# Performance work log

Hardware: AMD Instinct MI355X
Metric: run time of the kernel (lower is better)

The kernel has to match this reference:

```python
import jax, jax.numpy as jnp
import numpy as np

B, S, E, H = 2, 2048, 1024, 16
D = E // H  # head_dim = 64


def setup_inputs() -> dict:
    key = jax.random.key(0)
    k1, k2, k3 = jax.random.split(key, 3)
    scale = 0.02  # GPT-2 init scale
    return {
        "hidden_states": jax.random.normal(k1, (B, S, E), dtype=jnp.float32),
        "c_attn_w": jax.random.normal(k2, (E, 3 * E), dtype=jnp.float32) * scale,
        "c_attn_b": jnp.zeros((3 * E,), dtype=jnp.float32),
        "c_proj_w": jax.random.normal(k3, (E, E), dtype=jnp.float32) * scale,
        "c_proj_b": jnp.zeros((E,), dtype=jnp.float32),
    }


def reference(hidden_states, c_attn_w, c_attn_b, c_proj_w, c_proj_b):
    # Conv1D: x @ W + b  -> qkv [B, S, 3E]
    qkv = hidden_states @ c_attn_w + c_attn_b
    q, k, v = jnp.split(qkv, 3, axis=-1)

    # split heads -> [B, H, S, D]
    def split_heads(t):
        return t.reshape(B, S, H, D).transpose(0, 2, 1, 3)

    q, k, v = split_heads(q), split_heads(k), split_heads(v)

    # naive full attention: QK^T / sqrt(D) -> softmax -> @ V
    attn_weights = jnp.einsum("bhqd,bhkd->bhqk", q, k) / jnp.sqrt(
        jnp.asarray(D, dtype=q.dtype)
    )
    attn_weights = jax.nn.softmax(attn_weights, axis=-1)
    attn_output = jnp.einsum("bhqk,bhkd->bhqd", attn_weights, v)

    # merge heads -> [B, S, E], then output projection
    attn_output = attn_output.transpose(0, 2, 1, 3).reshape(B, S, E)
    attn_output = attn_output @ c_proj_w + c_proj_b
    return attn_output
```

## Files before the change

kernel.cpp:

```cpp
#include <hip/hip_runtime.h>

#define SEQ 2048
#define EMB 1024
#define KDIM 1024
#define CF 0.180336880111113f

typedef __attribute__((ext_vector_type(8))) short short8_t;
typedef __attribute__((ext_vector_type(4))) float floatx4;
typedef __attribute__((ext_vector_type(4))) unsigned short ushort4_t;

#define GLOAD16(gp, lp)                                                        \
  __builtin_amdgcn_global_load_lds(                                            \
      (const __attribute__((address_space(1))) void*)(gp),                     \
      (__attribute__((address_space(3))) void*)(lp), 16, 0, 0)

#define WGBAR()                                   \
  do {                                            \
    __asm__ __volatile__("" ::: "memory");        \
    __builtin_amdgcn_s_barrier();                 \
    __asm__ __volatile__("" ::: "memory");        \
  } while (0)

static __device__ __forceinline__ unsigned short f2bf(float x) {
  unsigned int u = __float_as_uint(x);
  return (unsigned short)((u + 0x7fffu + ((u >> 16) & 1u)) >> 16);
}

static __device__ __forceinline__ void tconv_tile(
    const float* __restrict__ W, unsigned short* __restrict__ T, int N, int K,
    int n0, int k0, int tid) {
  __shared__ float Tl[64][65];
  const int lx = tid & 15, ly = tid >> 4;
#pragma unroll
  for (int u = 0; u < 4; ++u) {
    int r = u * 16 + ly;
    float4 v = *(const float4*)&W[(size_t)(k0 + r) * N + n0 + lx * 4];
    Tl[r][lx * 4 + 0] = v.x;
    Tl[r][lx * 4 + 1] = v.y;
    Tl[r][lx * 4 + 2] = v.z;
    Tl[r][lx * 4 + 3] = v.w;
  }
  __syncthreads();
#pragma unroll
  for (int u = 0; u < 4; ++u) {
    int n = u * 16 + ly;
    ushort4_t h;
#pragma unroll
    for (int v = 0; v < 4; ++v) h[v] = f2bf(Tl[lx * 4 + v][n]);
    *(ushort4_t*)&T[(size_t)(n0 + n) * K + k0 + lx * 4] = h;
  }
}

__global__ __launch_bounds__(256) void prep(
    const float* __restrict__ hs, const float* __restrict__ caw,
    const float* __restrict__ cpw, unsigned short* __restrict__ hsb,
    unsigned short* __restrict__ w1t, unsigned short* __restrict__ w2t) {
  const int bid = blockIdx.x, tid = threadIdx.x;
  if (bid < 4096) {
    const int i = bid * 256 + tid;
    float4 v = *(const float4*)&hs[(size_t)i * 4];
    ushort4_t h = {f2bf(v.x), f2bf(v.y), f2bf(v.z), f2bf(v.w)};
    *(ushort4_t*)&hsb[(size_t)i * 4] = h;
  } else if (bid < 4864) {
    const int idx = bid - 4096;
    tconv_tile(caw, w1t, 3 * EMB, EMB, (idx % 48) * 64, (idx / 48) * 64, tid);
  } else {
    const int idx = bid - 4864;
    tconv_tile(cpw, w2t, EMB, EMB, (idx % 16) * 64, (idx / 16) * 64, tid);
  }
}

template <int MODE, int BN>
__global__ __launch_bounds__(256) void gemm_pl(
    const unsigned short* __restrict__ Ag, const unsigned short* __restrict__ Bg,
    const float* __restrict__ bias, float* __restrict__ outF,
    unsigned short* __restrict__ qk, unsigned short* __restrict__ vt) {
  __shared__ __attribute__((aligned(16))) unsigned short Ah[3][128 * 32];
  __shared__ __attribute__((aligned(16))) unsigned short Bh[3][BN * 32];
  const int NJ = BN / 32;

  const int tid = threadIdx.x;
  const int w = tid >> 6, lane = tid & 63;
  const int quad = lane >> 4, c = lane & 15;

  int bm, bn;
  {
    const int L = blockIdx.x, x = L & 7, g = L >> 3;
    if (MODE == 0) {
      bm = ((x & 1) * 16 + (g & 15)) * 128;
      bn = ((x >> 1) * 6 + (g >> 4)) * 128;
    } else {
      bm = ((x & 3) * 8 + (g & 7)) * 128;
      bn = ((x >> 2) * 8 + (g >> 3)) * 64;
    }
  }
  const int wm = (w >> 1) * 64, wn = (w & 1) * (BN / 2);

  const unsigned short* gsrc = (w < 2) ? Ag : Bg;
  const int lbo = (w < 2) ? (w & 1) * 64 * 32 : (w & 1) * (BN / 2) * 32;
  const int rbase = (w < 2) ? (bm + (w & 1) * 64) : (bn + (w & 1) * (BN / 2));
  const int nloads = (w < 2) ? 4 : (BN / 32);
  const int srow = lane >> 2;
  const int sblk = (lane & 3) ^ ((lane >> 3) & 3);
  const char* gp0 = (const char*)(gsrc + (size_t)(rbase + srow) * KDIM) + sblk * 16;

  floatx4 acc[4][NJ];
  const floatx4 z = {0.f, 0.f, 0.f, 0.f};
#pragma unroll
  for (int i = 0; i < 4; ++i)
#pragma unroll
    for (int j = 0; j < NJ; ++j) acc[i][j] = z;

  const int sw = (c >> 1) & 3;

#define STAGE_G(buf, kt)                                                       \
  do {                                                                         \
    unsigned short* ld = ((w < 2) ? Ah[buf] : Bh[buf]) + lbo;                  \
    const char* gp = gp0 + (size_t)(kt) * 64;                                  \
    for (int i_ = 0; i_ < nloads; ++i_)                                        \
      GLOAD16(gp + (size_t)i_ * 16 * (KDIM * 2), &ld[i_ * 512]);               \
  } while (0)

  STAGE_G(0, 0);
  STAGE_G(1, 1);

  for (int t = 0; t < 32; ++t) {
    if (BN == 128 || w < 2) {
      __asm__ __volatile__("s_waitcnt vmcnt(4)" ::: "memory");
    } else {
      __asm__ __volatile__("s_waitcnt vmcnt(2)" ::: "memory");
    }
    WGBAR();
    STAGE_G((t + 2) % 3, (t + 2) & 31);
    const unsigned short* Ac = Ah[t % 3];
    const unsigned short* Bc = Bh[t % 3];

    const int oct = (quad ^ sw) * 8;
    short8_t a[4], b[NJ];
#pragma unroll
    for (int i = 0; i < 4; ++i)
      a[i] = *(const short8_t*)&Ac[(wm + 16 * i + c) * 32 + oct];
#pragma unroll
    for (int j = 0; j < NJ; ++j)
      b[j] = *(const short8_t*)&Bc[(wn + 16 * j + c) * 32 + oct];
#pragma unroll
    for (int i = 0; i < 4; ++i)
#pragma unroll
      for (int j = 0; j < NJ; ++j)
        acc[i][j] = __builtin_amdgcn_mfma_f32_16x16x32_bf16(b[j], a[i], acc[i][j], 0, 0, 0);
  }
#undef STAGE_G

  __asm__ __volatile__("s_waitcnt vmcnt(0)" ::: "memory");

#pragma unroll
  for (int i = 0; i < 4; ++i) {
    const int row = bm + wm + 16 * i + c;
#pragma unroll
    for (int j = 0; j < NJ; ++j) {
      const int col0 = bn + wn + 16 * j + quad * 4;
      floatx4 v = acc[i][j] + *(const floatx4*)&bias[col0];
      if (MODE == 0) {
        if (col0 < 1024) v = v * CF;
        if (col0 < 2048) {
          ushort4_t pk = {f2bf(v[0]), f2bf(v[1]), f2bf(v[2]), f2bf(v[3])};
          *(ushort4_t*)&qk[(size_t)row * 2048 + col0] = pk;
        } else {
          const int c2 = col0 - 2048, hh = c2 >> 6, d0 = c2 & 63;
          const int bb = row >> 11, s = row & 2047;
          unsigned short* vb = &vt[((size_t)(bb * 16 + hh) * 64 + d0) * 2048 + s];
          vb[0 * 2048] = f2bf(v[0]);
          vb[1 * 2048] = f2bf(v[1]);
          vb[2 * 2048] = f2bf(v[2]);
          vb[3 * 2048] = f2bf(v[3]);
        }
      } else {
        *(floatx4*)&outF[(size_t)row * 1024 + col0] = v;
      }
    }
  }
}

static __device__ __forceinline__ void stage_kv(
    int w, int srow, int sblkg, const unsigned short* __restrict__ gK,
    const unsigned short* __restrict__ gV, unsigned short* Kbuf,
    unsigned short* Vbuf, int jt) {
  if (w < 2) {
    const unsigned short* g0 = gK + (size_t)(jt * 64 + w * 32 + srow) * 2048 + sblkg * 8;
    unsigned short* l0 = &Kbuf[(w * 32) * 64];
#pragma unroll
    for (int i = 0; i < 4; ++i) GLOAD16(g0 + (size_t)i * 8 * 2048, &l0[i * 512]);
  } else {
    const unsigned short* g0 = gV + (size_t)((w - 2) * 32 + srow) * 2048 + jt * 64 + sblkg * 8;
    unsigned short* l0 = &Vbuf[((w - 2) * 32) * 64];
#pragma unroll
    for (int i = 0; i < 4; ++i) GLOAD16(g0 + (size_t)i * 8 * 2048, &l0[i * 512]);
  }
}

__global__ __launch_bounds__(256) void attn6(
    const unsigned short* __restrict__ qk, const unsigned short* __restrict__ vt,
    unsigned short* __restrict__ ao) {
  __shared__ __attribute__((aligned(16))) unsigned short Ks[3][64 * 64];
  __shared__ __attribute__((aligned(16))) unsigned short Vs[3][64 * 64];
  __shared__ __attribute__((aligned(16))) unsigned short Ps[4][32 * 64];

  const int tid = threadIdx.x;
  const int w = tid >> 6, lane = tid & 63, quad = lane >> 4, c = lane & 15;
  const int q0 = blockIdx.x * 128, h = blockIdx.y, b = blockIdx.z;
  const int rk = c & 7;

  short8_t qf[2][2];
  {
    const size_t rb = (size_t)b * SEQ + q0 + w * 32;
#pragma unroll
    for (int mi = 0; mi < 2; ++mi) {
      const size_t qr = (rb + mi * 16 + c) * 2048 + h * 64 + quad * 8;
      qf[mi][0] = *(const short8_t*)&qk[qr];
      qf[mi][1] = *(const short8_t*)&qk[qr + 32];
    }
  }
  __asm__ __volatile__("s_waitcnt vmcnt(0)" ::: "memory");

  floatx4 O[2][4], Osum[2];
  const floatx4 z = {0.f, 0.f, 0.f, 0.f};
#pragma unroll
  for (int mi = 0; mi < 2; ++mi) {
    Osum[mi] = z;
#pragma unroll
    for (int dg = 0; dg < 4; ++dg) O[mi][dg] = z;
  }
  short8_t ones;
#pragma unroll
  for (int e = 0; e < 8; ++e) ones[e] = (short)0x3F80;

  const int srow = lane >> 3;
  const int sblkg = (lane & 7) ^ srow;
  const unsigned short* gK = qk + (size_t)b * SEQ * 2048 + 1024 + h * 64;
  const unsigned short* gV = vt + (size_t)(b * 16 + h) * 64 * 2048;
  unsigned short* myPs = Ps[w];

  stage_kv(w, srow, sblkg, gK, gV, Ks[0], Vs[0], 0);
  stage_kv(w, srow, sblkg, gK, gV, Ks[1], Vs[1], 1);

  for (int t = 0; t < 32; ++t) {
    __asm__ __volatile__("s_waitcnt vmcnt(4)" ::: "memory");
    WGBAR();
    stage_kv(w, srow, sblkg, gK, gV, Ks[(t + 2) % 3], Vs[(t + 2) % 3], (t + 2) & 31);
    const unsigned short* Kc = Ks[t % 3];
    const unsigned short* Vc = Vs[t % 3];

    floatx4 S[2][4];
#pragma unroll
    for (int mi = 0; mi < 2; ++mi)
#pragma unroll
      for (int jg = 0; jg < 4; ++jg) S[mi][jg] = z;
#pragma unroll
    for (int kd = 0; kd < 2; ++kd) {
      const int oct = ((4 * kd + quad) ^ rk) * 8;
#pragma unroll
      for (int jg = 0; jg < 4; ++jg) {
        short8_t kf = *(const short8_t*)&Kc[(jg * 16 + c) * 64 + oct];
#pragma unroll
        for (int mi = 0; mi < 2; ++mi)
          S[mi][jg] = __builtin_amdgcn_mfma_f32_16x16x32_bf16(kf, qf[mi][kd], S[mi][jg], 0, 0, 0);
      }
    }

#pragma unroll
    for (int mi = 0; mi < 2; ++mi) {
      const int qrow = (mi * 16 + c) * 64;
#pragma unroll
      for (int jg = 0; jg < 4; ++jg) {
        float p0 = __builtin_amdgcn_exp2f(S[mi][jg][0]);
        float p1 = __builtin_amdgcn_exp2f(S[mi][jg][1]);
        float p2 = __builtin_amdgcn_exp2f(S[mi][jg][2]);
        float p3 = __builtin_amdgcn_exp2f(S[mi][jg][3]);
        unsigned int pk01 = (__float_as_uint(p1) & 0xFFFF0000u) | (__float_as_uint(p0) >> 16);
        unsigned int pk23 = (__float_as_uint(p3) & 0xFFFF0000u) | (__float_as_uint(p2) >> 16);
        const int jp0 = 8 * jg + 2 * quad;
#pragma unroll
        for (int u = 0; u < 2; ++u) {
          const int jp = jp0 + u;
          const int off = ((jp >> 2) ^ rk) * 8 + (jp & 3) * 2;
          *(unsigned int*)&myPs[qrow + off] = u ? pk23 : pk01;
        }
      }
    }
    __asm__ __volatile__("s_waitcnt lgkmcnt(0)" ::: "memory");

#pragma unroll
    for (int kq = 0; kq < 2; ++kq) {
      const int oct = ((4 * kq + quad) ^ rk) * 8;
      short8_t pb[2];
#pragma unroll
      for (int mi = 0; mi < 2; ++mi) {
        pb[mi] = *(const short8_t*)&myPs[(mi * 16 + c) * 64 + oct];
        Osum[mi] = __builtin_amdgcn_mfma_f32_16x16x32_bf16(ones, pb[mi], Osum[mi], 0, 0, 0);
      }
#pragma unroll
      for (int dg = 0; dg < 4; ++dg) {
        short8_t vf = *(const short8_t*)&Vc[(dg * 16 + c) * 64 + oct];
#pragma unroll
        for (int mi = 0; mi < 2; ++mi)
          O[mi][dg] = __builtin_amdgcn_mfma_f32_16x16x32_bf16(vf, pb[mi], O[mi][dg], 0, 0, 0);
      }
    }
  }

  __asm__ __volatile__("s_waitcnt vmcnt(0)" ::: "memory");

#pragma unroll
  for (int mi = 0; mi < 2; ++mi) {
    const float inv = 1.0f / Osum[mi][0];
    const size_t row = (size_t)b * SEQ + q0 + w * 32 + mi * 16 + c;
#pragma unroll
    for (int dg = 0; dg < 4; ++dg) {
      ushort4_t ov = {f2bf(O[mi][dg][0] * inv), f2bf(O[mi][dg][1] * inv),
                      f2bf(O[mi][dg][2] * inv), f2bf(O[mi][dg][3] * inv)};
      *(ushort4_t*)&ao[row * EMB + h * 64 + dg * 16 + quad * 4] = ov;
    }
  }
}

extern "C" void kernel_launch(void* const* d_in, const int* in_sizes, int n_in,
                              void* d_out, int out_size, void* d_ws, size_t ws_size,
                              hipStream_t stream) {
  const float* hs = (const float*)d_in[0];
  const float* c_attn_w = (const float*)d_in[1];
  const float* c_attn_b = (const float*)d_in[2];
  const float* c_proj_w = (const float*)d_in[3];
  const float* c_proj_b = (const float*)d_in[4];
  float* out = (float*)d_out;

  char* ws = (char*)d_ws;
  unsigned short* hsb = (unsigned short*)(ws + 0);
  unsigned short* qk  = (unsigned short*)(ws + 8388608);
  unsigned short* vt  = (unsigned short*)(ws + 25165824);
  unsigned short* aob = (unsigned short*)(ws + 33554432);
  unsigned short* w1t = (unsigned short*)(ws + 41943040);
  unsigned short* w2t = (unsigned short*)(ws + 48234496);

  prep<<<5120, 256, 0, stream>>>(hs, c_attn_w, c_proj_w, hsb, w1t, w2t);
  gemm_pl<0, 128><<<768, 256, 0, stream>>>(hsb, w1t, c_attn_b, nullptr, qk, vt);
  attn6<<<dim3(16, 16, 2), 256, 0, stream>>>(qk, vt, aob);
  gemm_pl<2, 64><<<512, 256, 0, stream>>>(aob, w2t, c_proj_b, out, nullptr, nullptr);
}
```

Before: 183.4 us.

## Keep softmax probabilities in registers by permuting V layout in QKV epilogue

Removes the per-wave LDS round trip for the P tile by building the bf16 MFMA B-operand directly from the exp results held in registers. To make the register fragment order match, the QKV GEMM epilogue writes V^T with a permuted sequence index within each 64-key block, so the PV MFMA's k-ordering stays consistent. This saves LDS writes and reads plus a waitcnt per tile, and frees the Ps shared memory. The cost is a scattered store pattern in the V epilogue, and correctness depends on the permutation exactly matching the MFMA output layout.

```diff
diff --git a/kernel.cpp b/kernel.cpp
--- a/kernel.cpp
+++ b/kernel.cpp
@@ -8,6 +8,7 @@
 typedef __attribute__((ext_vector_type(8))) short short8_t;
 typedef __attribute__((ext_vector_type(4))) float floatx4;
 typedef __attribute__((ext_vector_type(4))) unsigned short ushort4_t;
+typedef __attribute__((ext_vector_type(4))) unsigned int uivec4;
 
 #define GLOAD16(gp, lp)                                                        \
   __builtin_amdgcn_global_load_lds(                                            \
@@ -24,6 +25,13 @@
 static __device__ __forceinline__ unsigned short f2bf(float x) {
   unsigned int u = __float_as_uint(x);
   return (unsigned short)((u + 0x7fffu + ((u >> 16) & 1u)) >> 16);
+}
+
+static __device__ __forceinline__ short8_t mk_pb(unsigned int a, unsigned int b,
+                                                 unsigned int c, unsigned int d) {
+  uivec4 t;
+  t[0] = a; t[1] = b; t[2] = c; t[3] = d;
+  return __builtin_bit_cast(short8_t, t);
 }
 
 static __device__ __forceinline__ void tconv_tile(
@@ -168,7 +176,10 @@
         } else {
           const int c2 = col0 - 2048, hh = c2 >> 6, d0 = c2 & 63;
           const int bb = row >> 11, s = row & 2047;
-          unsigned short* vb = &vt[((size_t)(bb * 16 + hh) * 64 + d0) * 2048 + s];
+          const int j = s & 63;
+          const int lam = (j & 0x20) | ((j & 0x0C) << 1) | ((j & 0x10) >> 2) | (j & 3);
+          const int sp = (s & ~63) | lam;
+          unsigned short* vb = &vt[((size_t)(bb * 16 + hh) * 64 + d0) * 2048 + sp];
           vb[0 * 2048] = f2bf(v[0]);
           vb[1 * 2048] = f2bf(v[1]);
           vb[2 * 2048] = f2bf(v[2]);
@@ -203,7 +214,6 @@
     unsigned short* __restrict__ ao) {
   __shared__ __attribute__((aligned(16))) unsigned short Ks[3][64 * 64];
   __shared__ __attribute__((aligned(16))) unsigned short Vs[3][64 * 64];
-  __shared__ __attribute__((aligned(16))) unsigned short Ps[4][32 * 64];
 
   const int tid = threadIdx.x;
   const int w = tid >> 6, lane = tid & 63, quad = lane >> 4, c = lane & 15;
@@ -238,7 +248,6 @@
   const int sblkg = (lane & 7) ^ srow;
   const unsigned short* gK = qk + (size_t)b * SEQ * 2048 + 1024 + h * 64;
   const unsigned short* gV = vt + (size_t)(b * 16 + h) * 64 * 2048;
-  unsigned short* myPs = Ps[w];
 
   stage_kv(w, srow, sblkg, gK, gV, Ks[0], Vs[0], 0);
   stage_kv(w, srow, sblkg, gK, gV, Ks[1], Vs[1], 1);
@@ -267,27 +276,18 @@
       }
     }
 
-#pragma unroll
-    for (int mi = 0; mi < 2; ++mi) {
-      const int qrow = (mi * 16 + c) * 64;
+    unsigned int pw[2][4][2];
+#pragma unroll
+    for (int mi = 0; mi < 2; ++mi)
 #pragma unroll
       for (int jg = 0; jg < 4; ++jg) {
         float p0 = __builtin_amdgcn_exp2f(S[mi][jg][0]);
         float p1 = __builtin_amdgcn_exp2f(S[mi][jg][1]);
         float p2 = __builtin_amdgcn_exp2f(S[mi][jg][2]);
         float p3 = __builtin_amdgcn_exp2f(S[mi][jg][3]);
-        unsigned int pk01 = (__float_as_uint(p1) & 0xFFFF0000u) | (__float_as_uint(p0) >> 16);
-        unsigned int pk23 = (__float_as_uint(p3) & 0xFFFF0000u) | (__float_as_uint(p2) >> 16);
-        const int jp0 = 8 * jg + 2 * quad;
-#pragma unroll
-        for (int u = 0; u < 2; ++u) {
-          const int jp = jp0 + u;
-          const int off = ((jp >> 2) ^ rk) * 8 + (jp & 3) * 2;
-          *(unsigned int*)&myPs[qrow + off] = u ? pk23 : pk01;
-        }
-      }
-    }
-    __asm__ __volatile__("s_waitcnt lgkmcnt(0)" ::: "memory");
+        pw[mi][jg][0] = (__float_as_uint(p1) & 0xFFFF0000u) | (__float_as_uint(p0) >> 16);
+        pw[mi][jg][1] = (__float_as_uint(p3) & 0xFFFF0000u) | (__float_as_uint(p2) >> 16);
+      }
 
 #pragma unroll
     for (int kq = 0; kq < 2; ++kq) {
@@ -295,7 +295,8 @@
       short8_t pb[2];
 #pragma unroll
       for (int mi = 0; mi < 2; ++mi) {
-        pb[mi] = *(const short8_t*)&myPs[(mi * 16 + c) * 64 + oct];
+        pb[mi] = mk_pb(pw[mi][2 * kq][0], pw[mi][2 * kq][1],
+                       pw[mi][2 * kq + 1][0], pw[mi][2 * kq + 1][1]);
         Osum[mi] = __builtin_amdgcn_mfma_f32_16x16x32_bf16(ones, pb[mi], Osum[mi], 0, 0, 0);
       }
 #pragma unroll
```

Result: no change. 181.0 us (-1.3%).
